# Kernel optimization log

Hardware: AMD Instinct MI355X
Metric: run time of the kernel (lower is better)

Reference implementation:

```python
import jax, jax.numpy as jnp
import numpy as np


def setup_inputs() -> dict:
    key = jax.random.key(0)
    ks = jax.random.split(key, 9)
    B, C, H, W = 4, 256, 64, 64
    Ci = C // 2
    s = 0.05  # keep activations numerically tame
    return {
        "x": jax.random.normal(ks[0], (B, C, H, W), jnp.float32),
        "w_g": jax.random.normal(ks[1], (Ci, C), jnp.float32) * s,
        "b_g": jax.random.normal(ks[2], (Ci,), jnp.float32) * s,
        "w_theta": jax.random.normal(ks[3], (Ci, C), jnp.float32) * s,
        "b_theta": jax.random.normal(ks[4], (Ci,), jnp.float32) * s,
        "w_phi": jax.random.normal(ks[5], (Ci, C), jnp.float32) * s,
        "b_phi": jax.random.normal(ks[6], (Ci,), jnp.float32) * s,
        "w_out": jax.random.normal(ks[7], (C, Ci), jnp.float32) * s,
        "b_out": jax.random.normal(ks[8], (C,), jnp.float32) * s,
    }


def reference(x, w_g, b_g, w_theta, b_theta, w_phi, b_phi, w_out, b_out):
    B, C, H, W = x.shape
    Ci = w_g.shape[0]
    N = H * W
    xr = x.reshape(B, C, N)  # flatten spatial dims

    def proj(w, b):  # 1x1 conv == per-pixel GEMM
        return jnp.einsum("oc,bcn->bon", w, xr) + b[None, :, None]

    g_x = proj(w_g, b_g)          # [B, Ci, N]
    theta_x = proj(w_theta, b_theta)
    phi_x = proj(w_phi, b_phi)

    scale = jnp.asarray(Ci, x.dtype) ** 0.5
    f = jnp.einsum("bci,bcj->bij", theta_x, phi_x) / scale  # [B, N, N]
    attn = jax.nn.softmax(f, axis=-1)

    # out[b,c,i] = sum_j g_x[b,c,j] * attn[b,i,j]
    out = jnp.einsum("bcj,bij->bci", g_x, attn)             # [B, Ci, N]
    y = jnp.einsum("oc,bcn->bon", w_out, out) + b_out[None, :, None]
    return y.reshape(B, C, H, W) + x
```

## Files before the change

### kernel.cpp

```cpp
#include <hip/hip_runtime.h>
#include <hip/hip_bf16.h>
#include <hip/hip_fp16.h>


typedef float f32x4 __attribute__((ext_vector_type(4)));
typedef float f32x16 __attribute__((ext_vector_type(16)));
typedef short s16x8 __attribute__((ext_vector_type(8)));

#define B_  4
#define C_  256
#define CI_ 128
#define N_  4096

#define OFF_Q    (8ull  << 20)
#define OFF_K    (12ull << 20)
#define OFF_G    (16ull << 20)
#define OFF_O    (20ull << 20)
#define OFF_WQK  (24ull << 20)
#define OFF_WG   (OFF_WQK + 131072)
#define OFF_WOUT (OFF_WG  + 65536)
#define OFF_BQK  (OFF_WOUT + 65536)
#define OFF_BG   (OFF_BQK + 1024)
#define OFF_BOUT (OFF_BG  + 512)
#define OFF_END  (OFF_BOUT + 1024)

__device__ inline f32x4 mfma16(s16x8 a, s16x8 b, f32x4 c) {
    return __builtin_amdgcn_mfma_f32_16x16x32_bf16(a, b, c, 0, 0, 0);
}
__device__ inline f32x16 mfma32f8(long a, long b, f32x16 c) {
    return __builtin_amdgcn_mfma_f32_32x32x16_fp8_fp8(a, b, c, 0, 0, 0);
}
__device__ inline s16x8 ld8(const __hip_bfloat16* p) { return *(const s16x8*)p; }
__device__ inline float b2f(short u) {
    return __uint_as_float(((unsigned int)(unsigned short)u) << 16);
}
__device__ inline unsigned int pk2(float a, float b) {
    __hip_bfloat162 h;
    h.x = __float2bfloat16(a); h.y = __float2bfloat16(b);
    return *(unsigned int*)&h;
}
__device__ inline unsigned char f2fp8(float v) {
    int r = __builtin_amdgcn_cvt_pk_fp8_f32(v, v, 0, false);
    return (unsigned char)(r & 0xff);
}
__device__ inline float fp8q(unsigned int byte) {
    union { unsigned short u; __half h; } cv;
    cv.u = (unsigned short)(((byte & 0x80u) << 8) | ((byte & 0x7fu) << 7));
    return __half2float(cv.h);
}
__device__ inline void gload_lds16(const void* g, void* l) {
    __builtin_amdgcn_global_load_lds(
        (const __attribute__((address_space(1))) unsigned int*)g,
        (__attribute__((address_space(3))) unsigned int*)l, 16, 0, 0);
}
__device__ inline float fexp2(float x) { return __builtin_amdgcn_exp2f(x); }

__global__ void prep_weights(const float* wg, const float* bg,
                             const float* wt, const float* bt,
                             const float* wp, const float* bp,
                             const float* wo, const float* bo, char* ws) {
    __hip_bfloat16* Wqk  = (__hip_bfloat16*)(ws + OFF_WQK);
    __hip_bfloat16* Wg   = (__hip_bfloat16*)(ws + OFF_WG);
    __hip_bfloat16* Wout = (__hip_bfloat16*)(ws + OFF_WOUT);
    float* Bqk  = (float*)(ws + OFF_BQK);
    float* Bg   = (float*)(ws + OFF_BG);
    float* Bout = (float*)(ws + OFF_BOUT);
    const float rs16 = 0.08838834764831845f * 1.4426950408889634f * 16.0f;
    int idx = blockIdx.x * 256 + threadIdx.x;
    if (idx < 65536) {
        int r = idx >> 8, c = idx & 255;
        float v = (r < 128) ? wt[r * 256 + c] * rs16 : wp[(r - 128) * 256 + c];
        Wqk[idx] = __float2bfloat16(v);
    }
    if (idx < 32768) {
        Wg[idx]   = __float2bfloat16(wg[idx]);
        Wout[idx] = __float2bfloat16(wo[idx]);
    }
    if (idx < 256) { Bqk[idx] = (idx < 128) ? bt[idx] * rs16 : bp[idx - 128]; Bout[idx] = bo[idx]; }
    if (idx < 128) Bg[idx] = bg[idx];
}

__global__ __launch_bounds__(256) void proj(const float* x, char* ws) {
    const __hip_bfloat16* Wqk = (const __hip_bfloat16*)(ws + OFF_WQK);
    const __hip_bfloat16* Wg  = (const __hip_bfloat16*)(ws + OFF_WG);
    const float* Bqk = (const float*)(ws + OFF_BQK);
    const float* Bg  = (const float*)(ws + OFF_BG);
    unsigned char* Qf = (unsigned char*)(ws + OFF_Q);
    unsigned char* Kt = (unsigned char*)(ws + OFF_K);
    unsigned char* Gt = (unsigned char*)(ws + OFF_G);

    __shared__ char at[32 * 512];

    int b = blockIdx.y, n0 = blockIdx.x * 32;
    int t = threadIdx.x;
    int w = t >> 6, l = t & 63, lr = l & 15, lg = l >> 4;

    {
        int n4 = (t & 7) * 4;
        int cp = t >> 3;
        const float* xb = x + ((size_t)b * C_) * N_ + n0 + n4;
#pragma unroll
        for (int p = 0; p < 4; p++) {
            int c0 = (p * 32 + cp) * 2;
            f32x4 vA = *(const f32x4*)(xb + (size_t)c0 * N_);
            f32x4 vB = *(const f32x4*)(xb + (size_t)(c0 + 1) * N_);
            int slot = c0 >> 3, coff = (c0 & 7) << 1;
#pragma unroll
            for (int i = 0; i < 4; i++) {
                int n = n4 + i;
                *(unsigned int*)(&at[n * 512 + ((slot ^ (n & 7)) << 4) + coff]) =
                    pk2(vA[i], vB[i]);
            }
        }
    }
    __syncthreads();

    f32x4 acc[4][2] = {};
    f32x4 accg[2][2] = {};
    int o0q = w * 64, o0g = w * 32;
#pragma unroll
    for (int kk = 0; kk < 8; kk++) {
        s16x8 a[2];
#pragma unroll
        for (int nf = 0; nf < 2; nf++) {
            int row = nf * 16 + lr;
            int s = (4 * kk + lg) ^ (row & 7);
            a[nf] = *(const s16x8*)(&at[row * 512 + s * 16]);
        }
#pragma unroll
        for (int of = 0; of < 4; of++) {
            s16x8 bb = ld8(Wqk + (size_t)(o0q + 16 * of + lr) * C_ + kk * 32 + lg * 8);
            acc[of][0] = mfma16(a[0], bb, acc[of][0]);
            acc[of][1] = mfma16(a[1], bb, acc[of][1]);
        }
#pragma unroll
        for (int og = 0; og < 2; og++) {
            s16x8 ag = ld8(Wg + (size_t)(o0g + 16 * og + lr) * C_ + kk * 32 + lg * 8);
            accg[og][0] = mfma16(ag, a[0], accg[og][0]);
            accg[og][1] = mfma16(ag, a[1], accg[og][1]);
        }
    }
#pragma unroll
    for (int of = 0; of < 4; of++) {
        int o = o0q + 16 * of + lr;
        float bias = Bqk[o];
#pragma unroll
        for (int nf = 0; nf < 2; nf++) {
#pragma unroll
            for (int i = 0; i < 4; i++) {
                int n = n0 + 16 * nf + lg * 4 + i;
                float v = acc[of][nf][i] + bias;
                unsigned char u8 = f2fp8(v);
                if (o < 128) {
                    Qf[((size_t)b * N_ + n) * 128 + o] = u8;
                } else {
                    int op = o - 128;
                    size_t a2 = (((size_t)b * (N_ / 32) + (n >> 5)) << 12) +
                                ((op >> 3) << 8) + ((n & 31) << 3) + (op & 7);
                    Kt[a2] = u8;
                }
            }
        }
    }
#pragma unroll
    for (int og = 0; og < 2; og++) {
#pragma unroll
        for (int i = 0; i < 4; i++) {
            int o = o0g + 16 * og + lg * 4 + i;
            float bias = Bg[o];
#pragma unroll
            for (int nf = 0; nf < 2; nf++) {
                int n = n0 + 16 * nf + lr;
                float v = accg[og][nf][i] + bias;
                size_t a3 = (((size_t)b * (N_ / 32) + (n >> 5)) << 12) +
                            (((n & 31) >> 3) << 10) + (o << 3) + (n & 7);
                Gt[a3] = f2fp8(v);
            }
        }
    }
}

__global__ __launch_bounds__(256, 4) void flashf8b(char* ws, int nchunk,
                                                   unsigned long long off_part,
                                                   unsigned long long off_ml) {
    const unsigned char* Qf = (const unsigned char*)(ws + OFF_Q);
    const unsigned char* Kt = (const unsigned char*)(ws + OFF_K);
    const unsigned char* Gt = (const unsigned char*)(ws + OFF_G);
    unsigned char* OP = (unsigned char*)(ws + off_part);
    float* ML = (float*)(ws + off_ml);

    __shared__ char kbuf[2][4096];
    __shared__ char vbuf[2][4096];

    int L = blockIdx.x;
    int npairs = B_ * nchunk;
    int pair = L % npairs, qt = L / npairs;
    int b = pair / nchunk, cz = pair % nchunk;
    int per = 128 / nchunk, rem = 128 % nchunk;
    int jb_t = per * cz + (cz < rem ? cz : rem);
    int sz_t = per + (cz < rem ? 1 : 0);
    int jb = jb_t << 5, je = jb + (sz_t << 5);

    int w = threadIdx.x >> 6, l = threadIdx.x & 63;
    int cl = l & 31, hi = l >> 5;
    int q0 = qt * 128 + w * 32;

    auto STAGE = [&](int pb_, int j0_) {
        {
            const char* src = (const char*)Kt +
                (((size_t)b * (N_ / 32) + (j0_ >> 5)) << 12) + w * 1024 + (l << 4);
            gload_lds16(src, &kbuf[pb_][w * 1024]);
        }
        {
            const char* src = (const char*)Gt +
                (((size_t)b * (N_ / 32) + (j0_ >> 5)) << 12) + w * 1024 + (l << 4);
            gload_lds16(src, &vbuf[pb_][w * 1024]);
        }
    };

    long qf[8];
    {
        const char* qrow = (const char*)Qf + ((size_t)b * N_ + q0 + cl) * 128 + hi * 8;
#pragma unroll
        for (int st = 0; st < 8; st++) qf[st] = *(const long*)(qrow + st * 16);
    }

    f32x16 oacc[4] = {};
    float m_i = 0.f, lsum = 0.f, negmc = 0.f;

    STAGE(0, jb);
    __syncthreads();
    int pb = 0;

    for (int j0 = jb; j0 < je; j0 += 32) {
        if (j0 + 32 < je) STAGE(pb ^ 1, j0 + 32);
        const char* kb = kbuf[pb];
        const char* vbb = vbuf[pb];
        f32x16 s = {};
        __builtin_amdgcn_s_setprio(1);
#pragma unroll
        for (int st = 0; st < 8; st++) {
            long kf = *(const long*)(kb + (((st << 1) + hi) << 8) + (cl << 3));
            s = mfma32f8(kf, qf[st], s);
        }
        __builtin_amdgcn_s_setprio(0);
        if (j0 == jb) {
            float t0 = fmaxf(fmaxf(s[0], s[1]), fmaxf(s[2], s[3]));
            float t1 = fmaxf(fmaxf(s[4], s[5]), fmaxf(s[6], s[7]));
            float t2 = fmaxf(fmaxf(s[8], s[9]), fmaxf(s[10], s[11]));
            float t3 = fmaxf(fmaxf(s[12], s[13]), fmaxf(s[14], s[15]));
            float tm = fmaxf(fmaxf(t0, t1), fmaxf(t2, t3));
            tm = fmaxf(tm, __shfl_xor(tm, 32));
            m_i = tm;
            negmc = -m_i * 0.0625f;
        }
#pragma unroll
        for (int r = 0; r < 16; r++) s[r] = fexp2(fmaf(s[r], 0.0625f, negmc));
        lsum += ((s[0] + s[1]) + (s[2] + s[3])) + ((s[4] + s[5]) + (s[6] + s[7]))
              + ((s[8] + s[9]) + (s[10] + s[11])) + ((s[12] + s[13]) + (s[14] + s[15]));
        long pa01[2];
        {
            int u0 = __builtin_amdgcn_cvt_pk_fp8_f32(s[0], s[1], 0, false);
            u0     = __builtin_amdgcn_cvt_pk_fp8_f32(s[2], s[3], u0, true);
            int u1 = __builtin_amdgcn_cvt_pk_fp8_f32(s[4], s[5], 0, false);
            u1     = __builtin_amdgcn_cvt_pk_fp8_f32(s[6], s[7], u1, true);
            pa01[0] = (long)(((unsigned long long)(unsigned int)u1 << 32) |
                             (unsigned int)u0);
            int u2 = __builtin_amdgcn_cvt_pk_fp8_f32(s[8], s[9], 0, false);
            u2     = __builtin_amdgcn_cvt_pk_fp8_f32(s[10], s[11], u2, true);
            int u3 = __builtin_amdgcn_cvt_pk_fp8_f32(s[12], s[13], 0, false);
            u3     = __builtin_amdgcn_cvt_pk_fp8_f32(s[14], s[15], u3, true);
            pa01[1] = (long)(((unsigned long long)(unsigned int)u3 << 32) |
                             (unsigned int)u2);
        }
        __builtin_amdgcn_s_setprio(1);
#pragma unroll
        for (int u = 0; u < 2; u++) {
            long pa = pa01[u];
#pragma unroll
            for (int cb = 0; cb < 4; cb++) {
                int c = cb * 32 + cl;
                unsigned int vlo = *(const unsigned int*)(vbb + ((u << 1) << 10) +
                                                          (c << 3) + (hi << 2));
                unsigned int vhi = *(const unsigned int*)(vbb + (((u << 1) | 1) << 10) +
                                                          (c << 3) + (hi << 2));
                long vf = (long)(((unsigned long long)vhi << 32) | vlo);
                oacc[cb] = mfma32f8(pa, vf, oacc[cb]);
            }
        }
        __builtin_amdgcn_s_setprio(0);
        __syncthreads();
        pb ^= 1;
    }
    lsum += __shfl_xor(lsum, 32);
#pragma unroll
    for (int cb = 0; cb < 4; cb++) {
#pragma unroll
        for (int r = 0; r < 16; r++) {
            int q = q0 + (r & 3) + 8 * (r >> 2) + 4 * hi;
            OP[((size_t)(cz * B_ + b) * N_ + q) * CI_ + cb * 32 + cl] =
                f2fp8(oacc[cb][r] * 0.0625f);
        }
    }
    if (l < 32) {
        size_t mi = ((size_t)(cz * B_ + b) * N_ + q0 + l) * 2;
        ML[mi] = m_i * 0.0625f;
        ML[mi + 1] = lsum;
    }
}

template <int NC>
__global__ __launch_bounds__(256) void combine(char* ws,
                                               unsigned long long off_part,
                                               unsigned long long off_ml) {
    const unsigned char* OP = (const unsigned char*)(ws + off_part);
    const float* ML = (const float*)(ws + off_ml);
    __hip_bfloat16* O = (__hip_bfloat16*)(ws + OFF_O);
    int idx = blockIdx.x * 256 + threadIdx.x;
    int cg = idx & 15, n = (idx >> 4) & (N_ - 1), b = idx >> 16;
    float mz[NC], lz[NC], M = -1e30f;
#pragma unroll
    for (int z = 0; z < NC; z++) {
        size_t mi = ((size_t)(z * B_ + b) * N_ + n) * 2;
        mz[z] = ML[mi]; lz[z] = ML[mi + 1];
        M = fmaxf(M, mz[z]);
    }
    float Lsum = 0.f, wz[NC];
#pragma unroll
    for (int z = 0; z < NC; z++) { wz[z] = fexp2(mz[z] - M); Lsum += lz[z] * wz[z]; }
    float inv = 4096.0f / Lsum;
    float o[8] = {};
#pragma unroll
    for (int z = 0; z < NC; z++) {
        unsigned long long v8 = *(const unsigned long long*)(
            OP + ((size_t)(z * B_ + b) * N_ + n) * CI_ + cg * 8);
        float wv = wz[z] * inv;
#pragma unroll
        for (int i = 0; i < 8; i++)
            o[i] += wv * fp8q((unsigned int)((v8 >> (8 * i)) & 0xffull));
    }
    s16x8 r;
#pragma unroll
    for (int i = 0; i < 8; i++) {
        __hip_bfloat16 h = __float2bfloat16(o[i]);
        r[i] = *(short*)&h;
    }
    *(s16x8*)(O + ((size_t)b * N_ + n) * CI_ + cg * 8) = r;
}

__global__ __launch_bounds__(256) void gemm_out(const float* x, char* ws, float* y) {
    const __hip_bfloat16* Ob = (const __hip_bfloat16*)(ws + OFF_O);
    const __hip_bfloat16* Wo = (const __hip_bfloat16*)(ws + OFF_WOUT);
    const float* Bout = (const float*)(ws + OFF_BOUT);
    int b = blockIdx.y;
    int w = threadIdx.x >> 6, l = threadIdx.x & 63, lr = l & 15, lg = l >> 4;
    int n0 = blockIdx.x * 32;
    int o0 = w * 64;
    f32x4 acc[4][2] = {};
#pragma unroll
    for (int kk = 0; kk < 4; kk++) {
        s16x8 bb[2];
#pragma unroll
        for (int nf = 0; nf < 2; nf++)
            bb[nf] = ld8(Ob + (size_t)(b * N_ + n0 + 16 * nf + lr) * CI_ + kk * 32 + lg * 8);
#pragma unroll
        for (int of = 0; of < 4; of++) {
            s16x8 a = ld8(Wo + (size_t)(o0 + 16 * of + lr) * CI_ + kk * 32 + lg * 8);
#pragma unroll
            for (int nf = 0; nf < 2; nf++)
                acc[of][nf] = mfma16(a, bb[nf], acc[of][nf]);
        }
    }
#pragma unroll
    for (int of = 0; of < 4; of++) {
#pragma unroll
        for (int i = 0; i < 4; i++) {
            int o = o0 + 16 * of + lg * 4 + i;
            float bias = Bout[o];
#pragma unroll
            for (int nf = 0; nf < 2; nf++) {
                int n = n0 + 16 * nf + lr;
                size_t idx = (size_t)(b * C_ + o) * N_ + n;
                y[idx] = acc[of][nf][i] + bias + x[idx];
            }
        }
    }
}

extern "C" void kernel_launch(void* const* d_in, const int* in_sizes, int n_in,
                              void* d_out, int out_size, void* d_ws, size_t ws_size,
                              hipStream_t stream) {
    const float* x  = (const float*)d_in[0];
    const float* wg = (const float*)d_in[1];
    const float* bg = (const float*)d_in[2];
    const float* wt = (const float*)d_in[3];
    const float* bt = (const float*)d_in[4];
    const float* wp = (const float*)d_in[5];
    const float* bp = (const float*)d_in[6];
    const float* wo = (const float*)d_in[7];
    const float* bo = (const float*)d_in[8];
    char* ws = (char*)d_ws;
    float* y = (float*)d_out;

    unsigned long long need8 = OFF_END + (32ull << 20) + (2ull << 20);
    unsigned long long need4 = OFF_END + (16ull << 20) + (1ull << 20);
    int nchunk;
    unsigned long long off_part, off_ml;
    if (ws_size >= need8) {
        nchunk = 8; off_part = OFF_END; off_ml = OFF_END + (32ull << 20);
    } else if (ws_size >= need4) {
        nchunk = 4; off_part = OFF_END; off_ml = OFF_END + (16ull << 20);
    } else {
        nchunk = 2; off_part = 0ull; off_ml = OFF_END;
    }

    prep_weights<<<256, 256, 0, stream>>>(wg, bg, wt, bt, wp, bp, wo, bo, ws);
    proj<<<dim3(128, 4), 256, 0, stream>>>(x, ws);
    flashf8b<<<dim3(32 * B_ * nchunk), 256, 0, stream>>>(ws, nchunk, off_part, off_ml);
    if (nchunk == 8)      combine<8><<<1024, 256, 0, stream>>>(ws, off_part, off_ml);
    else if (nchunk == 4) combine<4><<<1024, 256, 0, stream>>>(ws, off_part, off_ml);
    else                  combine<2><<<1024, 256, 0, stream>>>(ws, off_part, off_ml);
    gemm_out<<<dim3(128, 4), 256, 0, stream>>>(x, ws, y);
}
```

Baseline: 84.37 us.

## Fuse split-KV combine into output projection GEMM via LDS tile

Merges the combine kernel, which normalises and sums the fp8 partial attention outputs, into the output 1x1-conv GEMM. Each block combines 16 pixels into a swizzled bf16 tile in shared memory and then runs the MFMA projection plus bias and residual directly from it. This removes one kernel launch and the global write and re-read of the bf16 intermediate O. The cost is half the column tile per block (16 instead of 32), so each block re-reads the weights for less work.

Result: faster. 81.58 us (-3.3%).

```diff
diff --git a/kernel.cpp b/kernel.cpp
--- a/kernel.cpp
+++ b/kernel.cpp
@@ -15,7 +15,6 @@
 #define OFF_Q    (8ull  << 20)
 #define OFF_K    (12ull << 20)
 #define OFF_G    (16ull << 20)
-#define OFF_O    (20ull << 20)
 #define OFF_WQK  (24ull << 20)
 #define OFF_WG   (OFF_WQK + 131072)
 #define OFF_WOUT (OFF_WG  + 65536)
@@ -310,65 +309,63 @@
 }
 
 template <int NC>
-__global__ __launch_bounds__(256) void combine(char* ws,
-                                               unsigned long long off_part,
-                                               unsigned long long off_ml) {
+__global__ __launch_bounds__(256) void out_fused3(const float* x, char* ws, float* y,
+                                                  unsigned long long off_part,
+                                                  unsigned long long off_ml) {
     const unsigned char* OP = (const unsigned char*)(ws + off_part);
     const float* ML = (const float*)(ws + off_ml);
-    __hip_bfloat16* O = (__hip_bfloat16*)(ws + OFF_O);
-    int idx = blockIdx.x * 256 + threadIdx.x;
-    int cg = idx & 15, n = (idx >> 4) & (N_ - 1), b = idx >> 16;
-    float mz[NC], lz[NC], M = -1e30f;
-#pragma unroll
-    for (int z = 0; z < NC; z++) {
-        size_t mi = ((size_t)(z * B_ + b) * N_ + n) * 2;
-        mz[z] = ML[mi]; lz[z] = ML[mi + 1];
-        M = fmaxf(M, mz[z]);
-    }
-    float Lsum = 0.f, wz[NC];
-#pragma unroll
-    for (int z = 0; z < NC; z++) { wz[z] = fexp2(mz[z] - M); Lsum += lz[z] * wz[z]; }
-    float inv = 4096.0f / Lsum;
-    float o[8] = {};
-#pragma unroll
-    for (int z = 0; z < NC; z++) {
-        unsigned long long v8 = *(const unsigned long long*)(
-            OP + ((size_t)(z * B_ + b) * N_ + n) * CI_ + cg * 8);
-        float wv = wz[z] * inv;
-#pragma unroll
-        for (int i = 0; i < 8; i++)
-            o[i] += wv * fp8q((unsigned int)((v8 >> (8 * i)) & 0xffull));
-    }
-    s16x8 r;
-#pragma unroll
-    for (int i = 0; i < 8; i++) {
-        __hip_bfloat16 h = __float2bfloat16(o[i]);
-        r[i] = *(short*)&h;
-    }
-    *(s16x8*)(O + ((size_t)b * N_ + n) * CI_ + cg * 8) = r;
-}
-
-__global__ __launch_bounds__(256) void gemm_out(const float* x, char* ws, float* y) {
-    const __hip_bfloat16* Ob = (const __hip_bfloat16*)(ws + OFF_O);
     const __hip_bfloat16* Wo = (const __hip_bfloat16*)(ws + OFF_WOUT);
     const float* Bout = (const float*)(ws + OFF_BOUT);
+
+    __shared__ char oT[16 * 256];
+
     int b = blockIdx.y;
-    int w = threadIdx.x >> 6, l = threadIdx.x & 63, lr = l & 15, lg = l >> 4;
-    int n0 = blockIdx.x * 32;
+    int n0 = blockIdx.x * 16;
+    int t = threadIdx.x;
+
+    {
+        int nl = t >> 4;
+        int cg = t & 15;
+        int n = n0 + nl;
+        float mz[NC], lz[NC], M = -1e30f;
+#pragma unroll
+        for (int z = 0; z < NC; z++) {
+            size_t mi = ((size_t)(z * B_ + b) * N_ + n) * 2;
+            mz[z] = ML[mi]; lz[z] = ML[mi + 1];
+            M = fmaxf(M, mz[z]);
+        }
+        float Ls = 0.f, wz[NC];
+#pragma unroll
+        for (int z = 0; z < NC; z++) { wz[z] = fexp2(mz[z] - M); Ls += lz[z] * wz[z]; }
+        float inv = 4096.0f / Ls;
+        float o8[8] = {};
+#pragma unroll
+        for (int z = 0; z < NC; z++) {
+            unsigned long long v8 = *(const unsigned long long*)(
+                OP + ((size_t)(z * B_ + b) * N_ + n) * CI_ + cg * 8);
+            float wv = wz[z] * inv;
+#pragma unroll
+            for (int i = 0; i < 8; i++)
+                o8[i] += wv * fp8q((unsigned int)((v8 >> (8 * i)) & 0xffull));
+        }
+        union { unsigned int u[4]; s16x8 v; } r;
+#pragma unroll
+        for (int e = 0; e < 4; e++) r.u[e] = pk2(o8[2 * e], o8[2 * e + 1]);
+        *(s16x8*)(&oT[nl * 256 + ((cg ^ (nl & 7)) << 4)]) = r.v;
+    }
+    __syncthreads();
+
+    int w = t >> 6, l = t & 63, lr = l & 15, lg = l >> 4;
     int o0 = w * 64;
-    f32x4 acc[4][2] = {};
+    f32x4 acc[4] = {};
 #pragma unroll
     for (int kk = 0; kk < 4; kk++) {
-        s16x8 bb[2];
-#pragma unroll
-        for (int nf = 0; nf < 2; nf++)
-            bb[nf] = ld8(Ob + (size_t)(b * N_ + n0 + 16 * nf + lr) * CI_ + kk * 32 + lg * 8);
+        int slot = kk * 4 + lg;
+        s16x8 bb = *(const s16x8*)(&oT[lr * 256 + ((slot ^ (lr & 7)) << 4)]);
 #pragma unroll
         for (int of = 0; of < 4; of++) {
             s16x8 a = ld8(Wo + (size_t)(o0 + 16 * of + lr) * CI_ + kk * 32 + lg * 8);
-#pragma unroll
-            for (int nf = 0; nf < 2; nf++)
-                acc[of][nf] = mfma16(a, bb[nf], acc[of][nf]);
+            acc[of] = mfma16(a, bb, acc[of]);
         }
     }
 #pragma unroll
@@ -376,13 +373,9 @@
 #pragma unroll
         for (int i = 0; i < 4; i++) {
             int o = o0 + 16 * of + lg * 4 + i;
-            float bias = Bout[o];
-#pragma unroll
-            for (int nf = 0; nf < 2; nf++) {
-                int n = n0 + 16 * nf + lr;
-                size_t idx = (size_t)(b * C_ + o) * N_ + n;
-                y[idx] = acc[of][nf][i] + bias + x[idx];
-            }
+            int n = n0 + lr;
+            size_t idx = (size_t)(b * C_ + o) * N_ + n;
+            y[idx] = acc[of][i] + Bout[o] + x[idx];
         }
     }
 }
@@ -417,8 +410,10 @@
     prep_weights<<<256, 256, 0, stream>>>(wg, bg, wt, bt, wp, bp, wo, bo, ws);
     proj<<<dim3(128, 4), 256, 0, stream>>>(x, ws);
     flashf8b<<<dim3(32 * B_ * nchunk), 256, 0, stream>>>(ws, nchunk, off_part, off_ml);
-    if (nchunk == 8)      combine<8><<<1024, 256, 0, stream>>>(ws, off_part, off_ml);
-    else if (nchunk == 4) combine<4><<<1024, 256, 0, stream>>>(ws, off_part, off_ml);
-    else                  combine<2><<<1024, 256, 0, stream>>>(ws, off_part, off_ml);
-    gemm_out<<<dim3(128, 4), 256, 0, stream>>>(x, ws, y);
-}
+    if (nchunk == 8)
+        out_fused3<8><<<dim3(256, 4), 256, 0, stream>>>(x, ws, y, off_part, off_ml);
+    else if (nchunk == 4)
+        out_fused3<4><<<dim3(256, 4), 256, 0, stream>>>(x, ws, y, off_part, off_ml);
+    else
+        out_fused3<2><<<dim3(256, 4), 256, 0, stream>>>(x, ws, y, off_part, off_ml);
+}
```
